# Performance work log

Measured on AMD Instinct MI355X. Metric: run time of the kernel, lower is better.

Reference implementation:

```python
import jax, jax.numpy as jnp
import numpy as np

EPS = 1e-5  # torch LayerNorm default
NUM_HEADS = 16


def _ln(x, g, b):
    mu = x.mean(-1, keepdims=True)
    var = ((x - mu) ** 2).mean(-1, keepdims=True)
    return (x - mu) * jax.lax.rsqrt(var + EPS) * g + b


def _softmax1(logits):
    # softmax with an extra implicit zero logit appended on the last axis
    z = jnp.pad(logits, [(0, 0)] * (logits.ndim - 1) + [(0, 1)])
    return jax.nn.softmax(z, axis=-1)[..., :-1]


def setup_inputs() -> dict:
    key = jax.random.key(0)
    ks = jax.random.split(key, 8)
    B, N, C = 4, 1024, 1024
    Hd = 4 * C  # mlp hidden
    s = lambda k, shape, sc: (jax.random.normal(k, shape, jnp.float32) * sc)
    return {
        "x": s(ks[0], (B, N, C), 1.0),
        "mask": jax.random.bernoulli(ks[1], 0.1, (B, N, N)),  # True = masked
        "ln1_g": jnp.ones((C,), jnp.float32),
        "ln1_b": jnp.zeros((C,), jnp.float32),
        "qkv_w": s(ks[2], (3 * C, C), 0.02),
        "qkv_b": jnp.zeros((3 * C,), jnp.float32),
        "proj_w": s(ks[3], (C, C), 0.02),
        "proj_b": jnp.zeros((C,), jnp.float32),
        "ln2_g": jnp.ones((C,), jnp.float32),
        "ln2_b": jnp.zeros((C,), jnp.float32),
        "fc1_w": s(ks[4], (Hd, C), 0.02),
        "fc1_b": jnp.zeros((Hd,), jnp.float32),
        "fc2_w": s(ks[5], (C, Hd), 0.02),
        "fc2_b": jnp.zeros((C,), jnp.float32),
    }


def reference(x, mask, ln1_g, ln1_b, qkv_w, qkv_b, proj_w, proj_b,
              ln2_g, ln2_b, fc1_w, fc1_b, fc2_w, fc2_b):
    B, N, C = x.shape
    H = NUM_HEADS
    D = C // H
    scale = D ** (-0.5)
    # --- pre-norm attention ---
    h = _ln(x, ln1_g, ln1_b)
    qkv = (h @ qkv_w.T + qkv_b).reshape(B, N, 3, H, D).transpose(2, 0, 3, 1, 4)
    q, k, v = qkv[0], qkv[1], qkv[2]  # each [B,H,N,D]
    attn = jnp.einsum('bhqd,bhkd->bhqk', q, k) * scale
    attn = jnp.where(mask[:, None], -jnp.finfo(attn.dtype).max, attn)
    attn = _softmax1(attn)  # allow_zero_attn=True variant
    o = jnp.einsum('bhqk,bhkd->bqhd', attn, v).reshape(B, N, C)
    o = o @ proj_w.T + proj_b
    x = x + o
    # --- pre-norm MLP (exact GELU, matching torch nn.GELU default) ---
    h2 = _ln(x, ln2_g, ln2_b)
    m = jax.nn.gelu(h2 @ fc1_w.T + fc1_b, approximate=False)
    m = m @ fc2_w.T + fc2_b
    return x + m
```

## Files before the change

kernel.cpp:

```cpp
#include <hip/hip_runtime.h>
#include <hip/hip_bf16.h>
#include <cstdint>
#include <cstddef>

typedef __attribute__((ext_vector_type(4))) float f32x4;
typedef __attribute__((ext_vector_type(8))) short s16x8;
typedef __attribute__((ext_vector_type(4))) unsigned int u32x4;
typedef __attribute__((ext_vector_type(4))) unsigned short u16x4;

__device__ __forceinline__ unsigned short f2bf(float f) {
  union { float f; unsigned int u; } v; v.f = f;
  return (unsigned short)((v.u + 0x7fffu + ((v.u >> 16) & 1u)) >> 16);
}

__device__ __forceinline__ void gll16(const void* g, void* l) {
  __builtin_amdgcn_global_load_lds(
      (const __attribute__((address_space(1))) void*)g,
      (__attribute__((address_space(3))) void*)l, 16, 0, 0);
}

__global__ void mask_detect(const unsigned char* __restrict__ m, int* __restrict__ flag) {
  __shared__ int f;
  if (threadIdx.x == 0) f = 0;
  __syncthreads();
  unsigned int found = 0;
  for (int i = threadIdx.x * 16; i < 65536; i += 256 * 16) {
    u32x4 v = *(const u32x4*)(m + i);
    found |= (v.x & 0xFFFFFF00u) | (v.y & 0xFFFFFF00u) |
             (v.z & 0xFFFFFF00u) | (v.w & 0xFFFFFF00u);
  }
  if (found) atomicOr(&f, 1);
  __syncthreads();
  if (threadIdx.x == 0) *flag = f;
}

__global__ __launch_bounds__(256)
void ln_bf16(const float* __restrict__ x, const float* __restrict__ g,
             const float* __restrict__ bta, unsigned short* __restrict__ out) {
  const int row = blockIdx.x;
  const int t = threadIdx.x;
  const float* xr = x + (size_t)row * 1024;
  f32x4 v = *(const f32x4*)(xr + t * 4);
  float s  = v.x + v.y + v.z + v.w;
  float sq = v.x * v.x + v.y * v.y + v.z * v.z + v.w * v.w;
#pragma unroll
  for (int d = 1; d < 64; d <<= 1) { s += __shfl_xor(s, d, 64); sq += __shfl_xor(sq, d, 64); }
  __shared__ float ss[4], ssq[4];
  const int w = t >> 6;
  if ((t & 63) == 0) { ss[w] = s; ssq[w] = sq; }
  __syncthreads();
  s  = ss[0] + ss[1] + ss[2] + ss[3];
  sq = ssq[0] + ssq[1] + ssq[2] + ssq[3];
  const float mu  = s * (1.0f / 1024.0f);
  const float var = sq * (1.0f / 1024.0f) - mu * mu;
  const float rs  = rsqrtf(var + 1e-5f);
  f32x4 gv = *(const f32x4*)(g + t * 4);
  f32x4 bv = *(const f32x4*)(bta + t * 4);
  u16x4 o;
  o.x = f2bf((v.x - mu) * rs * gv.x + bv.x);
  o.y = f2bf((v.y - mu) * rs * gv.y + bv.y);
  o.z = f2bf((v.z - mu) * rs * gv.z + bv.z);
  o.w = f2bf((v.w - mu) * rs * gv.w + bv.w);
  *(u16x4*)(out + (size_t)row * 1024 + t * 4) = o;
}

__global__ __launch_bounds__(256)
void f32_to_bf16(const float* __restrict__ in, unsigned short* __restrict__ out, int n) {
  for (int i = (blockIdx.x * 256 + threadIdx.x) * 4; i < n; i += gridDim.x * 256 * 4) {
    f32x4 v = *(const f32x4*)(in + i);
    u16x4 o = { f2bf(v.x), f2bf(v.y), f2bf(v.z), f2bf(v.w) };
    *(u16x4*)(out + i) = o;
  }
}

__global__ __launch_bounds__(256)
void convert_weights(const float* __restrict__ w0, const float* __restrict__ w1,
                     const float* __restrict__ w2, const float* __restrict__ w3,
                     unsigned short* __restrict__ o0, unsigned short* __restrict__ o1,
                     unsigned short* __restrict__ o2, unsigned short* __restrict__ o3) {
  const int gid = blockIdx.x * 256 + threadIdx.x;
  for (int i = gid * 4; i < 12582912; i += gridDim.x * 256 * 4) {
    const float* src; unsigned short* dst; int off;
    if (i < 3145728)      { src = w0; dst = o0; off = i; }
    else if (i < 4194304) { src = w1; dst = o1; off = i - 3145728; }
    else if (i < 8388608) { src = w2; dst = o2; off = i - 4194304; }
    else                  { src = w3; dst = o3; off = i - 8388608; }
    f32x4 v = *(const f32x4*)(src + off);
    u16x4 o = { f2bf(v.x), f2bf(v.y), f2bf(v.z), f2bf(v.w) };
    *(u16x4*)(dst + off) = o;
  }
}

template<int EPI, int NW>
__global__ __launch_bounds__(256)
void gemm_bt(const unsigned short* __restrict__ A, const unsigned short* __restrict__ Bw,
             const float* __restrict__ bias, const float* __restrict__ resid,
             void* __restrict__ Cout, int M, int N, int K) {
  constexpr int BN = 32 * NW;
  __shared__ unsigned short As[2][128 * 64];
  __shared__ unsigned short Bs[2][BN * 64];
  const int tid = threadIdx.x;
  const int bx = blockIdx.x;
  const int by = blockIdx.y;
  const int w = tid >> 6, l = tid & 63;
  const int wr = w >> 1, wc = w & 1;
  const int lr = l & 15, lk = l >> 4;

  f32x4 acc[4][NW] = {};
  const int row0A = by * 128, row0B = bx * BN;

  auto stage = [&](int buf, int kt) {
#pragma unroll
    for (int it = 0; it < 4; ++it) {
      const int c = it * 256 + tid;
      const int r = c >> 3, c8 = (c & 7) * 8;
      gll16(A + (size_t)(row0A + r) * K + kt + c8, &As[buf][c * 8]);
      if (it < NW)
        gll16(Bw + (size_t)(row0B + r) * K + kt + c8, &Bs[buf][c * 8]);
    }
  };

  stage(0, 0);
  asm volatile("s_waitcnt vmcnt(0)" ::: "memory");
  __syncthreads();

  const int nsteps = K >> 6;
  for (int t = 0; t < nsteps; ++t) {
    const int cur = t & 1;
    if (t + 1 < nsteps) stage(cur ^ 1, (t + 1) * 64);
    const unsigned short* Ac = As[cur];
    const unsigned short* Bc = Bs[cur];
#pragma unroll
    for (int ks = 0; ks < 2; ++ks) {
      s16x8 af[4], bfr[NW];
#pragma unroll
      for (int m = 0; m < 4; ++m)
        af[m] = *(const s16x8*)&Ac[(wr * 64 + m * 16 + lr) * 64 + ks * 32 + lk * 8];
#pragma unroll
      for (int n = 0; n < NW; ++n)
        bfr[n] = *(const s16x8*)&Bc[(wc * (BN / 2) + n * 16 + lr) * 64 + ks * 32 + lk * 8];
#pragma unroll
      for (int m = 0; m < 4; ++m)
#pragma unroll
        for (int n = 0; n < NW; ++n)
          acc[m][n] = __builtin_amdgcn_mfma_f32_16x16x32_bf16(af[m], bfr[n], acc[m][n], 0, 0, 0);
    }
    if (t + 1 < nsteps) {
      asm volatile("s_waitcnt vmcnt(0)" ::: "memory");
      __syncthreads();
    }
  }
#pragma unroll
  for (int m = 0; m < 4; ++m) {
#pragma unroll
    for (int n = 0; n < NW; ++n) {
      const int col = bx * BN + wc * (BN / 2) + n * 16 + lr;
      const float bval = bias[col];
#pragma unroll
      for (int r2 = 0; r2 < 4; ++r2) {
        const int row = by * 128 + wr * 64 + m * 16 + lk * 4 + r2;
        float vv = acc[m][n][r2] + bval;
        const size_t idx = (size_t)row * N + col;
        if (EPI == 0) {
          ((unsigned short*)Cout)[idx] = f2bf(vv);
        } else if (EPI == 1) {
          const float t2 = vv * (1.5957691216f + 0.0713548163f * vv * vv);
          const float ge = vv / (1.0f + __expf(-t2));
          ((unsigned short*)Cout)[idx] = f2bf(ge);
        } else {
          ((float*)Cout)[idx] = vv + resid[idx];
        }
      }
    }
  }
}

__global__ __launch_bounds__(256, 4)
void attn2(const unsigned short* __restrict__ qkv, const void* __restrict__ maskp,
           const int* __restrict__ flag, unsigned short* __restrict__ o_ws) {
  __shared__ unsigned short Qs[64 * 64];
  __shared__ unsigned short Ks[64 * 64];
  __shared__ unsigned short Vts[64 * 64];
  __shared__ unsigned short Ps[4][16 * 64];

  const int tid = threadIdx.x;
  const int orig = blockIdx.x;
  const int swzb = (orig & 7) * 128 + (orig >> 3);
  const int bh = swzb >> 4, qt = swzb & 15;
  const int b = bh >> 4, h = bh & 15;
  const int q0 = qt * 64;
  const int w = tid >> 6, l = tid & 63;
  const int lr = l & 15, lk = l >> 4;
  const size_t rowbase = (size_t)b * 1024;
  const int qoff = h * 64, koff = 1024 + h * 64, voff = 2048 + h * 64;

#pragma unroll
  for (int it = 0; it < 2; ++it) {
    const int c = it * 256 + tid;
    const int r = c >> 3, j0 = c & 7;
    const int jsrc = j0 ^ (r & 7);
    gll16(qkv + (rowbase + q0 + r) * 3072 + qoff + jsrc * 8, Qs + c * 8);
  }
  const int mask_is_byte = *flag;
  const int qrow_g = q0 + w * 16 + lr;
  const unsigned char* mrow_b = (const unsigned char*)maskp + ((size_t)b * 1024 + qrow_g) * 1024;
  const int* mrow_i = (const int*)maskp + ((size_t)b * 1024 + qrow_g) * 1024;

  const int np = tid & 31, dg = tid >> 5;

  float m_r = 0.f, l_r = 1.f;
  f32x4 acc_o[4] = {};

  for (int nt = 0; nt < 16; ++nt) {
    const int n0 = nt * 64;
    const unsigned short* vsrc = qkv + (rowbase + n0 + 2 * np) * 3072 + voff + dg * 8;
    u32x4 va = *(const u32x4*)vsrc;
    u32x4 vb = *(const u32x4*)(vsrc + 3072);
    unsigned int mb[4];
    if (mask_is_byte) {
#pragma unroll
      for (int n = 0; n < 4; ++n)
        mb[n] = *(const unsigned int*)(mrow_b + n0 + n * 16 + lk * 4);
    } else {
#pragma unroll
      for (int n = 0; n < 4; ++n) {
        u32x4 t4 = *(const u32x4*)(mrow_i + n0 + n * 16 + lk * 4);
        mb[n] = (t4.x ? 1u : 0u) | (t4.y ? 0x100u : 0u) |
                (t4.z ? 0x10000u : 0u) | (t4.w ? 0x1000000u : 0u);
      }
    }
    __syncthreads();
#pragma unroll
    for (int it = 0; it < 2; ++it) {
      const int c = it * 256 + tid;
      const int r = c >> 3, j0 = c & 7;
      const int jsrc = j0 ^ (r & 7);
      gll16(qkv + (rowbase + n0 + r) * 3072 + koff + jsrc * 8, Ks + c * 8);
    }
    {
      const unsigned short* ea = (const unsigned short*)&va;
      const unsigned short* eb = (const unsigned short*)&vb;
#pragma unroll
      for (int j = 0; j < 8; ++j) {
        const int d = dg * 8 + j;
        const unsigned int pv = (unsigned int)ea[j] | ((unsigned int)eb[j] << 16);
        const int byte = (d * 128 + np * 4) ^ ((d & 7) << 4);
        *(unsigned int*)((char*)Vts + byte) = pv;
      }
    }
    asm volatile("s_waitcnt vmcnt(0)" ::: "memory");
    __syncthreads();

    f32x4 s_acc[4] = {};
#pragma unroll
    for (int ks = 0; ks < 2; ++ks) {
      const int cb = ks * 64 + lk * 16;
      const s16x8 qf = *(const s16x8*)((char*)Qs + (((w * 16 + lr) * 128 + cb) ^ ((lr & 7) << 4)));
#pragma unroll
      for (int n = 0; n < 4; ++n) {
        const s16x8 kf = *(const s16x8*)((char*)Ks + (((n * 16 + lr) * 128 + cb) ^ ((lr & 7) << 4)));
        s_acc[n] = __builtin_amdgcn_mfma_f32_16x16x32_bf16(kf, qf, s_acc[n], 0, 0, 0);
      }
    }
    float pmax = -3.0e38f;
#pragma unroll
    for (int n = 0; n < 4; ++n)
#pragma unroll
      for (int r2 = 0; r2 < 4; ++r2) {
        float s = s_acc[n][r2] * 0.125f;
        if ((mb[n] >> (8 * r2)) & 0xff) s = -3.0e38f;
        s_acc[n][r2] = s;
        pmax = fmaxf(pmax, s);
      }
    pmax = fmaxf(pmax, __shfl_xor(pmax, 16, 64));
    pmax = fmaxf(pmax, __shfl_xor(pmax, 32, 64));
    const float mnew = fmaxf(m_r, pmax);
    const float resc = __expf(m_r - mnew);
    m_r = mnew;
    float psum = 0.f;
    unsigned int pk[4][2];
#pragma unroll
    for (int n = 0; n < 4; ++n)
#pragma unroll
      for (int h2 = 0; h2 < 2; ++h2) {
        const float p0 = __expf(s_acc[n][2 * h2]     - mnew);
        const float p1 = __expf(s_acc[n][2 * h2 + 1] - mnew);
        psum += p0 + p1;
        pk[n][h2] = (unsigned int)f2bf(p0) | ((unsigned int)f2bf(p1) << 16);
      }
    psum += __shfl_xor(psum, 16, 64);
    psum += __shfl_xor(psum, 32, 64);
    l_r = l_r * resc + psum;
    char* psw = (char*)&Ps[w][0];
#pragma unroll
    for (int n = 0; n < 4; ++n)
#pragma unroll
      for (int h2 = 0; h2 < 2; ++h2) {
        const int byte = (lr * 128 + n * 32 + lk * 8 + h2 * 4) ^ ((lr & 7) << 4);
        *(unsigned int*)(psw + byte) = pk[n][h2];
      }
    float rs4[4];
#pragma unroll
    for (int r2 = 0; r2 < 4; ++r2)
      rs4[r2] = __shfl(resc, (l & 48) | (lk * 4 + r2), 64);
#pragma unroll
    for (int dn = 0; dn < 4; ++dn)
#pragma unroll
      for (int r2 = 0; r2 < 4; ++r2) acc_o[dn][r2] *= rs4[r2];
#pragma unroll
    for (int ks = 0; ks < 2; ++ks) {
      const int cb = ks * 64 + lk * 16;
      const s16x8 ap = *(const s16x8*)(psw + ((lr * 128 + cb) ^ ((lr & 7) << 4)));
#pragma unroll
      for (int dn = 0; dn < 4; ++dn) {
        const s16x8 bv = *(const s16x8*)((char*)Vts + (((dn * 16 + lr) * 128 + cb) ^ ((lr & 7) << 4)));
        acc_o[dn] = __builtin_amdgcn_mfma_f32_16x16x32_bf16(ap, bv, acc_o[dn], 0, 0, 0);
      }
    }
  }
  const float linv = 1.0f / l_r;
  float li4[4];
#pragma unroll
  for (int r2 = 0; r2 < 4; ++r2)
    li4[r2] = __shfl(linv, (l & 48) | (lk * 4 + r2), 64);
#pragma unroll
  for (int dn = 0; dn < 4; ++dn)
#pragma unroll
    for (int r2 = 0; r2 < 4; ++r2) {
      const int qrow = q0 + w * 16 + lk * 4 + r2;
      const int dcol = h * 64 + dn * 16 + lr;
      o_ws[(rowbase + qrow) * 1024 + dcol] = f2bf(acc_o[dn][r2] * li4[r2]);
    }
}

extern "C" void kernel_launch(void* const* d_in, const int* in_sizes, int n_in,
                              void* d_out, int out_size, void* d_ws, size_t ws_size,
                              hipStream_t stream) {
  const float* x      = (const float*)d_in[0];
  const void*  maskp  = d_in[1];
  const float* ln1_g  = (const float*)d_in[2];
  const float* ln1_b  = (const float*)d_in[3];
  const float* qkv_w  = (const float*)d_in[4];
  const float* qkv_b  = (const float*)d_in[5];
  const float* proj_w = (const float*)d_in[6];
  const float* proj_b = (const float*)d_in[7];
  const float* ln2_g  = (const float*)d_in[8];
  const float* ln2_b  = (const float*)d_in[9];
  const float* fc1_w  = (const float*)d_in[10];
  const float* fc1_b  = (const float*)d_in[11];
  const float* fc2_w  = (const float*)d_in[12];
  const float* fc2_b  = (const float*)d_in[13];
  float* out = (float*)d_out;

  char* ws = (char*)d_ws;
  int* flag            = (int*)ws;
  unsigned short* bufA = (unsigned short*)(ws + 256);
  unsigned short* bufH = (unsigned short*)(ws + 256 + 33554432);
  unsigned short* bufO = (unsigned short*)(ws + 256 + 33554432 + 8388608);
  float* bufX1         = (float*)(ws + 256 + 33554432 + 2 * 8388608);
  char* wbase          = ws + 256 + 33554432 + 2 * 8388608 + 16777216;

  mask_detect<<<1, 256, 0, stream>>>((const unsigned char*)maskp, flag);

  const bool bigws = ws_size >= (size_t)92274944;
  if (bigws) {
    unsigned short* W0 = (unsigned short*)wbase;
    unsigned short* W1 = (unsigned short*)(wbase + 6291456);
    unsigned short* W2 = (unsigned short*)(wbase + 8388608);
    unsigned short* W3 = (unsigned short*)(wbase + 16777216);
    convert_weights<<<4096, 256, 0, stream>>>(qkv_w, proj_w, fc1_w, fc2_w, W0, W1, W2, W3);
    ln_bf16<<<4096, 256, 0, stream>>>(x, ln1_g, ln1_b, bufH);
    gemm_bt<0, 4><<<dim3(24, 32), 256, 0, stream>>>(bufH, W0, qkv_b, nullptr, bufA, 4096, 3072, 1024);
    attn2<<<1024, 256, 0, stream>>>(bufA, maskp, flag, bufO);
    gemm_bt<2, 2><<<dim3(16, 32), 256, 0, stream>>>(bufO, W1, proj_b, x, bufX1, 4096, 1024, 1024);
    ln_bf16<<<4096, 256, 0, stream>>>(bufX1, ln2_g, ln2_b, bufH);
    gemm_bt<1, 4><<<dim3(32, 32), 256, 0, stream>>>(bufH, W2, fc1_b, nullptr, bufA, 4096, 4096, 1024);
    gemm_bt<2, 2><<<dim3(16, 32), 256, 0, stream>>>(bufA, W3, fc2_b, bufX1, out, 4096, 1024, 4096);
  } else {
    unsigned short* bufW = (unsigned short*)wbase;
    ln_bf16<<<4096, 256, 0, stream>>>(x, ln1_g, ln1_b, bufH);
    f32_to_bf16<<<2048, 256, 0, stream>>>(qkv_w, bufW, 3072 * 1024);
    gemm_bt<0, 4><<<dim3(24, 32), 256, 0, stream>>>(bufH, bufW, qkv_b, nullptr, bufA, 4096, 3072, 1024);
    attn2<<<1024, 256, 0, stream>>>(bufA, maskp, flag, bufO);
    f32_to_bf16<<<2048, 256, 0, stream>>>(proj_w, bufW, 1024 * 1024);
    gemm_bt<2, 2><<<dim3(16, 32), 256, 0, stream>>>(bufO, bufW, proj_b, x, bufX1, 4096, 1024, 1024);
    ln_bf16<<<4096, 256, 0, stream>>>(bufX1, ln2_g, ln2_b, bufH);
    f32_to_bf16<<<2048, 256, 0, stream>>>(fc1_w, bufW, 4096 * 1024);
    gemm_bt<1, 4><<<dim3(32, 32), 256, 0, stream>>>(bufH, bufW, fc1_b, nullptr, bufA, 4096, 4096, 1024);
    f32_to_bf16<<<2048, 256, 0, stream>>>(fc2_w, bufW, 1024 * 4096);
    gemm_bt<2, 2><<<dim3(16, 32), 256, 0, stream>>>(bufA, bufW, fc2_b, bufX1, out, 4096, 1024, 4096);
  }
}
```

Before: 413.7 us.

## Add 256x256 swizzled-LDS GEMM for QKV/FC1 and XCD-aware block remapping

Adds a new 512-thread GEMM kernel with 256x256 tiles and XOR-swizzled LDS, using split-phase staging and s_setprio around the MFMA bursts, for the QKV and FC1 projections. The existing GEMM now takes a 1D grid with an XCD-aware block remap, and the proj/fc2 GEMMs switch from BN=64 to BN=128 tiles. The aim is more operand reuse per byte loaded, fewer LDS bank conflicts and better L2 locality per XCD. The trade-off is fewer blocks (192 and 256 on the big GEMMs), one block per CU and higher register pressure.

```diff
diff --git a/kernel.cpp b/kernel.cpp
--- a/kernel.cpp
+++ b/kernel.cpp
@@ -17,6 +17,12 @@
   __builtin_amdgcn_global_load_lds(
       (const __attribute__((address_space(1))) void*)g,
       (__attribute__((address_space(3))) void*)l, 16, 0, 0);
+}
+
+__device__ __forceinline__ int xcd_swz(int id, int nwg) {
+  const int q = nwg >> 3, r = nwg & 7;
+  const int xcd = id & 7, i = id >> 3;
+  return ((xcd < r) ? xcd * (q + 1) : r * (q + 1) + (xcd - r) * q) + i;
 }
 
 __global__ void mask_detect(const unsigned char* __restrict__ m, int* __restrict__ flag) {
@@ -91,17 +97,145 @@
   }
 }
 
+template<int EPI>
+__global__ __launch_bounds__(512, 1)
+void gemm256(const unsigned short* __restrict__ A, const unsigned short* __restrict__ Bw,
+             const float* __restrict__ bias, void* __restrict__ Cout,
+             int M, int N, int K, int nbx) {
+  __shared__ unsigned short As[2][256 * 64];
+  __shared__ unsigned short Bs[2][256 * 64];
+  const int tid = threadIdx.x;
+  const int swz = xcd_swz(blockIdx.x, gridDim.x);
+  const int bx = swz % nbx, by = swz / nbx;
+
+  const int w = tid >> 6, l = tid & 63;
+  const int wr = w >> 2, wc = w & 3;
+  const int lr = l & 15, lk = l >> 4;
+  const int row0A = by * 256, row0B = bx * 256;
+
+  f32x4 acc[8][4] = {};
+
+  auto stageA = [&](int slot, int kt) {
+#pragma unroll
+    for (int ra = 0; ra < 4; ++ra) {
+      const int c = ra * 512 + tid;
+      const int rr = c >> 3, j0 = c & 7;
+      gll16(A + (size_t)(row0A + rr) * K + kt + (j0 ^ (rr & 7)) * 8, &As[slot][c * 8]);
+    }
+  };
+  auto stageB = [&](int slot, int kt) {
+#pragma unroll
+    for (int ra = 0; ra < 4; ++ra) {
+      const int c = ra * 512 + tid;
+      const int rr = c >> 3, j0 = c & 7;
+      gll16(Bw + (size_t)(row0B + rr) * K + kt + (j0 ^ (rr & 7)) * 8, &Bs[slot][c * 8]);
+    }
+  };
+  auto rdA = [&](int slot, int m, int ks) -> s16x8 {
+    const int row = wr * 128 + m * 16 + lr;
+    const int byte = (row * 128 + ks * 64 + lk * 16) ^ ((row & 7) << 4);
+    return *(const s16x8*)((const char*)&As[slot][0] + byte);
+  };
+  auto rdB = [&](int slot, int n, int ks) -> s16x8 {
+    const int row = wc * 64 + n * 16 + lr;
+    const int byte = (row * 128 + ks * 64 + lk * 16) ^ ((row & 7) << 4);
+    return *(const s16x8*)((const char*)&Bs[slot][0] + byte);
+  };
+
+  stageA(0, 0); stageB(0, 0);
+  asm volatile("s_waitcnt vmcnt(0)" ::: "memory");
+  __syncthreads();
+
+  const int nt = K >> 6;
+  s16x8 af[4][2], b01[2][2], b23[2][2];
+  for (int t = 0; t < nt; ++t) {
+    const int cur = t & 1;
+    const int ktn = (t + 1 < nt) ? (t + 1) * 64 : 0;
+#pragma unroll
+    for (int m = 0; m < 4; ++m) { af[m][0] = rdA(cur, m, 0); af[m][1] = rdA(cur, m, 1); }
+#pragma unroll
+    for (int n = 0; n < 2; ++n) { b01[n][0] = rdB(cur, n, 0); b01[n][1] = rdB(cur, n, 1); }
+    stageA(cur ^ 1, ktn);
+    __builtin_amdgcn_s_setprio(1);
+#pragma unroll
+    for (int m = 0; m < 4; ++m)
+#pragma unroll
+      for (int n = 0; n < 2; ++n)
+#pragma unroll
+        for (int ks = 0; ks < 2; ++ks)
+          acc[m][n] = __builtin_amdgcn_mfma_f32_16x16x32_bf16(af[m][ks], b01[n][ks], acc[m][n], 0, 0, 0);
+    __builtin_amdgcn_s_setprio(0);
+    __syncthreads();
+#pragma unroll
+    for (int n = 0; n < 2; ++n) { b23[n][0] = rdB(cur, n + 2, 0); b23[n][1] = rdB(cur, n + 2, 1); }
+    stageB(cur ^ 1, ktn);
+    __builtin_amdgcn_s_setprio(1);
+#pragma unroll
+    for (int m = 0; m < 4; ++m)
+#pragma unroll
+      for (int n = 0; n < 2; ++n)
+#pragma unroll
+        for (int ks = 0; ks < 2; ++ks)
+          acc[m][n + 2] = __builtin_amdgcn_mfma_f32_16x16x32_bf16(af[m][ks], b23[n][ks], acc[m][n + 2], 0, 0, 0);
+    __builtin_amdgcn_s_setprio(0);
+    __syncthreads();
+#pragma unroll
+    for (int m = 0; m < 4; ++m) { af[m][0] = rdA(cur, m + 4, 0); af[m][1] = rdA(cur, m + 4, 1); }
+    __builtin_amdgcn_s_setprio(1);
+#pragma unroll
+    for (int m = 0; m < 4; ++m)
+#pragma unroll
+      for (int n = 0; n < 2; ++n)
+#pragma unroll
+        for (int ks = 0; ks < 2; ++ks)
+          acc[m + 4][n + 2] = __builtin_amdgcn_mfma_f32_16x16x32_bf16(af[m][ks], b23[n][ks], acc[m + 4][n + 2], 0, 0, 0);
+    __builtin_amdgcn_s_setprio(0);
+    __syncthreads();
+    __builtin_amdgcn_s_setprio(1);
+#pragma unroll
+    for (int m = 0; m < 4; ++m)
+#pragma unroll
+      for (int n = 0; n < 2; ++n)
+#pragma unroll
+        for (int ks = 0; ks < 2; ++ks)
+          acc[m + 4][n] = __builtin_amdgcn_mfma_f32_16x16x32_bf16(af[m][ks], b01[n][ks], acc[m + 4][n], 0, 0, 0);
+    __builtin_amdgcn_s_setprio(0);
+    asm volatile("s_waitcnt vmcnt(0)" ::: "memory");
+    __syncthreads();
+  }
+#pragma unroll
+  for (int m = 0; m < 8; ++m) {
+#pragma unroll
+    for (int n = 0; n < 4; ++n) {
+      const int col = bx * 256 + wc * 64 + n * 16 + lr;
+      const float bval = bias[col];
+#pragma unroll
+      for (int r2 = 0; r2 < 4; ++r2) {
+        const int row = by * 256 + wr * 128 + m * 16 + lk * 4 + r2;
+        float vv = acc[m][n][r2] + bval;
+        const size_t idx = (size_t)row * N + col;
+        if (EPI == 0) {
+          ((unsigned short*)Cout)[idx] = f2bf(vv);
+        } else {
+          const float t2 = vv * (1.5957691216f + 0.0713548163f * vv * vv);
+          ((unsigned short*)Cout)[idx] = f2bf(vv / (1.0f + __expf(-t2)));
+        }
+      }
+    }
+  }
+}
+
 template<int EPI, int NW>
 __global__ __launch_bounds__(256)
 void gemm_bt(const unsigned short* __restrict__ A, const unsigned short* __restrict__ Bw,
              const float* __restrict__ bias, const float* __restrict__ resid,
-             void* __restrict__ Cout, int M, int N, int K) {
+             void* __restrict__ Cout, int M, int N, int K, int nbx) {
   constexpr int BN = 32 * NW;
   __shared__ unsigned short As[2][128 * 64];
   __shared__ unsigned short Bs[2][BN * 64];
   const int tid = threadIdx.x;
-  const int bx = blockIdx.x;
-  const int by = blockIdx.y;
+  const int swz = xcd_swz(blockIdx.x, gridDim.x);
+  const int bx = swz % nbx, by = swz / nbx;
   const int w = tid >> 6, l = tid & 63;
   const int wr = w >> 1, wc = w & 1;
   const int lr = l & 15, lk = l >> 4;
@@ -165,8 +299,7 @@
           ((unsigned short*)Cout)[idx] = f2bf(vv);
         } else if (EPI == 1) {
           const float t2 = vv * (1.5957691216f + 0.0713548163f * vv * vv);
-          const float ge = vv / (1.0f + __expf(-t2));
-          ((unsigned short*)Cout)[idx] = f2bf(ge);
+          ((unsigned short*)Cout)[idx] = f2bf(vv / (1.0f + __expf(-t2)));
         } else {
           ((float*)Cout)[idx] = vv + resid[idx];
         }
@@ -370,24 +503,24 @@
     unsigned short* W3 = (unsigned short*)(wbase + 16777216);
     convert_weights<<<4096, 256, 0, stream>>>(qkv_w, proj_w, fc1_w, fc2_w, W0, W1, W2, W3);
     ln_bf16<<<4096, 256, 0, stream>>>(x, ln1_g, ln1_b, bufH);
-    gemm_bt<0, 4><<<dim3(24, 32), 256, 0, stream>>>(bufH, W0, qkv_b, nullptr, bufA, 4096, 3072, 1024);
+    gemm256<0><<<192, 512, 0, stream>>>(bufH, W0, qkv_b, bufA, 4096, 3072, 1024, 12);
     attn2<<<1024, 256, 0, stream>>>(bufA, maskp, flag, bufO);
-    gemm_bt<2, 2><<<dim3(16, 32), 256, 0, stream>>>(bufO, W1, proj_b, x, bufX1, 4096, 1024, 1024);
+    gemm_bt<2, 4><<<256, 256, 0, stream>>>(bufO, W1, proj_b, x, bufX1, 4096, 1024, 1024, 8);
     ln_bf16<<<4096, 256, 0, stream>>>(bufX1, ln2_g, ln2_b, bufH);
-    gemm_bt<1, 4><<<dim3(32, 32), 256, 0, stream>>>(bufH, W2, fc1_b, nullptr, bufA, 4096, 4096, 1024);
-    gemm_bt<2, 2><<<dim3(16, 32), 256, 0, stream>>>(bufA, W3, fc2_b, bufX1, out, 4096, 1024, 4096);
+    gemm256<1><<<256, 512, 0, stream>>>(bufH, W2, fc1_b, bufA, 4096, 4096, 1024, 16);
+    gemm_bt<2, 4><<<256, 256, 0, stream>>>(bufA, W3, fc2_b, bufX1, out, 4096, 1024, 4096, 8);
   } else {
     unsigned short* bufW = (unsigned short*)wbase;
     ln_bf16<<<4096, 256, 0, stream>>>(x, ln1_g, ln1_b, bufH);
     f32_to_bf16<<<2048, 256, 0, stream>>>(qkv_w, bufW, 3072 * 1024);
-    gemm_bt<0, 4><<<dim3(24, 32), 256, 0, stream>>>(bufH, bufW, qkv_b, nullptr, bufA, 4096, 3072, 1024);
+    gemm256<0><<<192, 512, 0, stream>>>(bufH, bufW, qkv_b, bufA, 4096, 3072, 1024, 12);
     attn2<<<1024, 256, 0, stream>>>(bufA, maskp, flag, bufO);
     f32_to_bf16<<<2048, 256, 0, stream>>>(proj_w, bufW, 1024 * 1024);
-    gemm_bt<2, 2><<<dim3(16, 32), 256, 0, stream>>>(bufO, bufW, proj_b, x, bufX1, 4096, 1024, 1024);
+    gemm_bt<2, 4><<<256, 256, 0, stream>>>(bufO, bufW, proj_b, x, bufX1, 4096, 1024, 1024, 8);
     ln_bf16<<<4096, 256, 0, stream>>>(bufX1, ln2_g, ln2_b, bufH);
     f32_to_bf16<<<2048, 256, 0, stream>>>(fc1_w, bufW, 4096 * 1024);
-    gemm_bt<1, 4><<<dim3(32, 32), 256, 0, stream>>>(bufH, bufW, fc1_b, nullptr, bufA, 4096, 4096, 1024);
+    gemm256<1><<<256, 512, 0, stream>>>(bufH, bufW, fc1_b, bufA, 4096, 4096, 1024, 16);
     f32_to_bf16<<<2048, 256, 0, stream>>>(fc2_w, bufW, 1024 * 4096);
-    gemm_bt<2, 2><<<dim3(16, 32), 256, 0, stream>>>(bufA, bufW, fc2_b, bufX1, out, 4096, 1024, 4096);
-  }
-}
+    gemm_bt<2, 4><<<256, 256, 0, stream>>>(bufA, bufW, fc2_b, bufX1, out, 4096, 1024, 4096, 8);
+  }
+}
```

Result: no change. 409.6 us (-1.0%).
